# Kernel tuning notes

Hardware: AMD Instinct MI355X
Metric: run time of the kernel (lower is better)

## Reference

```python
import jax, jax.numpy as jnp
import numpy as np

N_NODES = 100000
N_EDGES = 1600000
NFEAT = 128
NHID = 128


def setup_inputs() -> dict:
    key = jax.random.key(0)
    k1, k2, k3, k4 = jax.random.split(key, 4)
    x = jax.random.normal(k1, (N_NODES, NFEAT), dtype=jnp.float32)
    edge_index = jax.random.randint(k2, (2, N_EDGES), 0, N_NODES, dtype=jnp.int64)
    # GCNConv params (glorot-style scale)
    W1 = jax.random.normal(k3, (NFEAT, NHID), dtype=jnp.float32) * (1.0 / np.sqrt(NFEAT))
    b1 = jnp.zeros((NHID,), dtype=jnp.float32)
    return {"x": x, "edge_index": edge_index, "W1": W1, "b1": b1}


def gcn_conv(x, edge_index, W, b):
    # PyG GCNConv: out = D^{-1/2} (A + I) D^{-1/2} (x W) + b
    n = x.shape[0]
    loop = jnp.arange(n, dtype=edge_index.dtype)
    src = jnp.concatenate([edge_index[0], loop])  # message sources
    dst = jnp.concatenate([edge_index[1], loop])  # aggregation targets
    deg = jax.ops.segment_sum(jnp.ones_like(dst, dtype=x.dtype), dst, num_segments=n)
    dinv = jnp.where(deg > 0, jax.lax.rsqrt(deg), 0.0)
    norm = dinv[src] * dinv[dst]  # [E+N]
    h = x @ W  # [N, nhid]
    msg = h[src] * norm[:, None]  # gather + scale, [E+N, nhid]
    out = jax.ops.segment_sum(msg, dst, num_segments=n) + b
    return out


def reference(x, edge_index, W1, b1):
    # forward = gc1(x, edge_index) followed by dropout (identity in eval mode)
    return gcn_conv(x, edge_index, W1, b1)
```

## Files before the change

kernel.cpp:

```cpp
#include <hip/hip_runtime.h>
#include <math.h>


#define N_NODES 100000
#define N_EDGES 1600000
#define NF 128
#define LDW 136

#define BSHIFT 7
#define BNODES 128
#define NBUCK 782
#define ECAP 2432
#define CHUNK 4096
#define NCHUNK 391
#define GEMM_BLOCKS 1563

typedef short bf16x8 __attribute__((ext_vector_type(8)));
typedef float f32x4  __attribute__((ext_vector_type(4)));
typedef unsigned short u16;

__device__ inline u16 f2bf(float f) {
    unsigned int u = __float_as_uint(f);
    return (u16)((u + 0x7fffu + ((u >> 16) & 1u)) >> 16);
}

__device__ inline f32x4 unpk4u(unsigned int u) {
    f32x4 r;
    r[0] = (float)(u & 0xffu);
    r[1] = (float)((u >> 8) & 0xffu);
    r[2] = (float)((u >> 16) & 0xffu);
    r[3] = (float)(u >> 24);
    return r;
}

__global__ __launch_bounds__(256) void prep_kernel(const float* __restrict__ W,
                                                   u16* __restrict__ Wimg,
                                                   int* __restrict__ bcur) {
    const int t = threadIdx.x;
    if (blockIdx.x == 0)
        for (int b = t; b < NBUCK; b += 256) bcur[b] = 0;
    for (int idx = blockIdx.x * 256 + t; idx < NF * NF; idx += 16 * 256) {
        int n = idx >> 7, k = idx & 127;
        Wimg[n * LDW + k] = f2bf(W[k * NF + n]);
    }
}

__global__ __launch_bounds__(256, 4) void fused1_kernel(const float* __restrict__ x,
                                                        const u16* __restrict__ Wimg,
                                                        signed char* __restrict__ h8,
                                                        float* __restrict__ rscale,
                                                        const int* __restrict__ ei,
                                                        int* __restrict__ bcur,
                                                        unsigned int* __restrict__ ebuf) {
    __shared__ __align__(16) char smem[39040];
    const int t = threadIdx.x;

    if (blockIdx.x < NCHUNK) {
        unsigned int* ed = (unsigned int*)smem;
        unsigned int* es = (unsigned int*)(smem + 16384);
        int* cnt = (int*)(smem + 32768);
        int* cur = (int*)(smem + 32768 + 3136);
        const int c = blockIdx.x;
        for (int b = t; b < NBUCK; b += 256) cnt[b] = 0;
        const int e0 = c * CHUNK;
        #pragma unroll 4
        for (int it = 0; it < CHUNK / 256; ++it) {
            int k = it * 256 + t, e = e0 + k;
            if (e < N_EDGES) {
                ed[k] = (unsigned int)ei[N_EDGES + e];
                es[k] = (unsigned int)ei[e];
            } else ed[k] = 0xFFFFFFFFu;
        }
        __syncthreads();
        #pragma unroll 4
        for (int it = 0; it < CHUNK / 256; ++it) {
            unsigned int d = ed[it * 256 + t];
            if (d != 0xFFFFFFFFu) atomicAdd(&cnt[d >> BSHIFT], 1);
        }
        __syncthreads();
        for (int b = t; b < NBUCK; b += 256) {
            int v = cnt[b];
            cur[b] = b * ECAP + (v ? atomicAdd(&bcur[b], v) : 0);
        }
        __syncthreads();
        #pragma unroll 4
        for (int it = 0; it < CHUNK / 256; ++it) {
            int k = it * 256 + t;
            unsigned int d = ed[k];
            if (d != 0xFFFFFFFFu) {
                int pos = atomicAdd(&cur[d >> BSHIFT], 1);
                ebuf[pos] = ((d & (BNODES - 1u)) << 17) | es[k];
            }
        }
        return;
    }

    const int gb = blockIdx.x - NCHUNK;
    const int lane = t & 63;
    const int w = t >> 6;
    const int quad = lane >> 4;
    const int m = lane & 15;
    const int rowbase = gb * 64;
    const int r0 = w * 16;
    const int arow = rowbase + r0 + m;
    const bool rv = arow < N_NODES;
    const float4* x4 = (const float4*)x;

    u16* Wt = (u16*)smem;
    for (int idx = t; idx < (NF * LDW * 2) / 16; idx += 256)
        ((uint4*)Wt)[idx] = ((const uint4*)Wimg)[idx];

    float4 xr[8];
    #pragma unroll
    for (int kt = 0; kt < 4; ++kt) {
        if (rv) {
            xr[2 * kt]     = x4[arow * 32 + kt * 8 + quad * 2];
            xr[2 * kt + 1] = x4[arow * 32 + kt * 8 + quad * 2 + 1];
        } else {
            xr[2 * kt] = make_float4(0.f, 0.f, 0.f, 0.f);
            xr[2 * kt + 1] = make_float4(0.f, 0.f, 0.f, 0.f);
        }
    }
    __syncthreads();

    f32x4 acc[8];
    #pragma unroll
    for (int nt = 0; nt < 8; ++nt) acc[nt] = (f32x4){0.f, 0.f, 0.f, 0.f};

    #pragma unroll
    for (int kt = 0; kt < 4; ++kt) {
        bf16x8 a;
        a[0] = (short)f2bf(xr[2 * kt].x);     a[1] = (short)f2bf(xr[2 * kt].y);
        a[2] = (short)f2bf(xr[2 * kt].z);     a[3] = (short)f2bf(xr[2 * kt].w);
        a[4] = (short)f2bf(xr[2 * kt + 1].x); a[5] = (short)f2bf(xr[2 * kt + 1].y);
        a[6] = (short)f2bf(xr[2 * kt + 1].z); a[7] = (short)f2bf(xr[2 * kt + 1].w);
        #pragma unroll
        for (int nt = 0; nt < 8; ++nt) {
            bf16x8 bb = *(const bf16x8*)&Wt[(nt * 16 + m) * LDW + kt * 32 + quad * 8];
            acc[nt] = __builtin_amdgcn_mfma_f32_16x16x32_bf16(a, bb, acc[nt], 0, 0, 0);
        }
    }

    float rmax[4];
    #pragma unroll
    for (int r = 0; r < 4; ++r) {
        float mx = 0.f;
        #pragma unroll
        for (int nt = 0; nt < 8; ++nt) mx = fmaxf(mx, fabsf(acc[nt][r]));
        #pragma unroll
        for (int off = 1; off < 16; off <<= 1) mx = fmaxf(mx, __shfl_xor(mx, off));
        rmax[r] = fmaxf(mx, 1e-20f);
    }

    __syncthreads();
    char* xs8 = smem;
    #pragma unroll
    for (int r = 0; r < 4; ++r) {
        const float inv = 127.f / rmax[r];
        const int row = r0 + quad * 4 + r;
        #pragma unroll
        for (int nt = 0; nt < 8; ++nt) {
            int q = __float2int_rn(acc[nt][r] * inv) + 128;
            xs8[row * 144 + nt * 16 + m] = (char)q;
        }
        if (m == 0) {
            int grow = rowbase + row;
            if (grow < N_NODES) rscale[grow] = rmax[r] * (1.f / 127.f);
        }
    }
    __syncthreads();

    for (int it = 0; it < 2; ++it) {
        int linear = it * 256 + t;
        int row = linear >> 3, seg = linear & 7;
        int grow = rowbase + row;
        if (grow < N_NODES) {
            uint4 v = *(const uint4*)&xs8[row * 144 + seg * 16];
            ((uint4*)h8)[grow * 8 + seg] = v;
        }
    }
}

__global__ __launch_bounds__(256) void fill3_kernel(unsigned int* __restrict__ ebuf,
                                                    const int* __restrict__ bcur,
                                                    const float* __restrict__ rscale,
                                                    float* __restrict__ combo,
                                                    int4* __restrict__ nodetab) {
    __shared__ unsigned int lde[ECAP];
    __shared__ int lcnt[BNODES];
    __shared__ int lsc[BNODES];
    __shared__ int lcur[BNODES];
    const int t = threadIdx.x, bkt = blockIdx.x;
    const int cnt = min(bcur[bkt], ECAP);
    const int gbase = bkt * ECAP;
    if (t < BNODES) lcnt[t] = 0;
    __syncthreads();
    for (int e = t; e < cnt; e += 256) {
        unsigned int p = ebuf[gbase + e];
        lde[e] = p;
        atomicAdd(&lcnt[p >> 17], 1);
    }
    __syncthreads();
    if (t < BNODES) lsc[t] = lcnt[t];
    __syncthreads();
    #pragma unroll
    for (int off = 1; off < BNODES; off <<= 1) {
        int v = (t < BNODES) ? lsc[t] : 0;
        int add = (t >= off && t < BNODES) ? lsc[t - off] : 0;
        __syncthreads();
        if (t < BNODES) lsc[t] = v + add;
        __syncthreads();
    }
    if (t < BNODES) {
        int c = lcnt[t];
        int startp = gbase + lsc[t] - c;
        lcur[t] = startp;
        int n = (bkt << BSHIFT) + t;
        if (n < N_NODES) {
            float dv = rsqrtf((float)c + 1.0f);
            float cb = dv * rscale[n];
            combo[n] = cb;
            nodetab[n] = make_int4(startp, c, __float_as_int(dv), __float_as_int(cb));
        }
    }
    __syncthreads();
    for (int e = t; e < cnt; e += 256) {
        unsigned int p = lde[e];
        int pos = atomicAdd(&lcur[p >> 17], 1);
        ebuf[pos] = p & 0x1ffffu;
    }
}

__global__ __launch_bounds__(256) void agg_kernel(const signed char* __restrict__ h8,
                                                  const float* __restrict__ combo,
                                                  const int4* __restrict__ nodetab,
                                                  const unsigned int* __restrict__ slot,
                                                  const float* __restrict__ b,
                                                  float* __restrict__ out) {
    const int wave = threadIdx.x >> 6;
    const int lane = threadIdx.x & 63;
    const int i = blockIdx.x * 4 + wave;
    if (i >= N_NODES) return;

    const int4 ni = nodetab[i];
    const int start = ni.x;
    const int m = ni.y;
    const float di = __int_as_float(ni.z);
    const float ci = __int_as_float(ni.w);
    const int half = lane >> 5;
    const int col = lane & 31;

    const unsigned int* h4 = (const unsigned int*)h8;
    f32x4 acc0 = {0.f, 0.f, 0.f, 0.f};
    f32x4 acc1 = {0.f, 0.f, 0.f, 0.f};
    float ws = 0.f;

    for (int base = 0; base < m; base += 64) {
        const int mm = min(m - base, 64);
        int   s_l  = (lane < mm) ? (int)slot[start + base + lane] : 0;
        float cw_l = (lane < mm) ? combo[s_l] : 0.0f;
        const int mu = (mm + 7) & ~7;
        for (int j = 0; j < mu; j += 8) {
            int sj0 = __shfl(s_l, j + 0 + half);
            int sj1 = __shfl(s_l, j + 2 + half);
            int sj2 = __shfl(s_l, j + 4 + half);
            int sj3 = __shfl(s_l, j + 6 + half);
            float wj0 = __shfl(cw_l, j + 0 + half);
            float wj1 = __shfl(cw_l, j + 2 + half);
            float wj2 = __shfl(cw_l, j + 4 + half);
            float wj3 = __shfl(cw_l, j + 6 + half);
            unsigned int u0 = h4[sj0 * 32 + col];
            unsigned int u1 = h4[sj1 * 32 + col];
            unsigned int u2 = h4[sj2 * 32 + col];
            unsigned int u3 = h4[sj3 * 32 + col];
            ws += wj0 + wj1 + wj2 + wj3;
            acc0 += unpk4u(u0) * wj0;
            acc1 += unpk4u(u1) * wj1;
            acc0 += unpk4u(u2) * wj2;
            acc1 += unpk4u(u3) * wj3;
        }
    }

    f32x4 acc = acc0 + acc1;
    #pragma unroll
    for (int c = 0; c < 4; ++c) acc[c] += __shfl_xor(acc[c], 32);
    ws += __shfl_xor(ws, 32);

    if (lane < 32) {
        unsigned int uv = h4[i * 32 + col];
        f32x4 hv = unpk4u(uv);
        float4 bb = ((const float4*)b)[col];
        const float corr = 128.f * (ws + ci);
        float4 o;
        o.x = bb.x + di * (acc[0] + ci * hv[0] - corr);
        o.y = bb.y + di * (acc[1] + ci * hv[1] - corr);
        o.z = bb.z + di * (acc[2] + ci * hv[2] - corr);
        o.w = bb.w + di * (acc[3] + ci * hv[3] - corr);
        ((float4*)out)[i * 32 + col] = o;
    }
}

extern "C" void kernel_launch(void* const* d_in, const int* in_sizes, int n_in,
                              void* d_out, int out_size, void* d_ws, size_t ws_size,
                              hipStream_t stream) {
    const float* x  = (const float*)d_in[0];
    const int*   ei = (const int*)d_in[1];
    const float* W  = (const float*)d_in[2];
    const float* b  = (const float*)d_in[3];
    float* out = (float*)d_out;

    signed char* h8 = (signed char*)d_ws;
    float* rscale = (float*)d_ws + 3300000;
    float* combo  = (float*)d_ws + 3500000;
    int4*  nodetab = (int4*)((int*)d_ws + 3700000);
    int*   bcur   = (int*)d_ws + 4150000;
    u16*   Wimg   = (u16*)((int*)d_ws + 4200000);
    unsigned int* ebuf = (unsigned int*)d_ws + 4300000;

    prep_kernel<<<16, 256, 0, stream>>>(W, Wimg, bcur);
    fused1_kernel<<<NCHUNK + GEMM_BLOCKS, 256, 0, stream>>>(x, Wimg, h8, rscale,
                                                            ei, bcur, ebuf);
    fill3_kernel<<<NBUCK, 256, 0, stream>>>(ebuf, bcur, rscale, combo, nodetab);
    agg_kernel<<<(N_NODES + 3) / 4, 256, 0, stream>>>(h8, combo, nodetab, ebuf, b, out);
}
```

Before: 191.9 us.

## Precompute per-edge source weights into interleaved slot buffer, split fill kernel

Node degrees are now counted with global atomics during edge bucketing. The fill stage is split into two kernels: one prefix-scans degrees to build the node table, the other sorts the edges in place and writes (source, combo weight) pairs. The aggregation kernel then reads the weight next to each source index, which removes its dependent random gather of combo per edge. In exchange there are 1.6M extra global atomics, a memset, one more kernel launch, a doubled slot stride and a smaller bucket capacity (ECAP), which raises the overflow risk for crowded buckets.

```diff
diff --git a/kernel.cpp b/kernel.cpp
--- a/kernel.cpp
+++ b/kernel.cpp
@@ -10,7 +10,7 @@
 #define BSHIFT 7
 #define BNODES 128
 #define NBUCK 782
-#define ECAP 2432
+#define ECAP 2304
 #define CHUNK 4096
 #define NCHUNK 391
 #define GEMM_BLOCKS 1563
@@ -51,7 +51,8 @@
                                                         float* __restrict__ rscale,
                                                         const int* __restrict__ ei,
                                                         int* __restrict__ bcur,
-                                                        unsigned int* __restrict__ ebuf) {
+                                                        int* __restrict__ deg,
+                                                        unsigned int* __restrict__ buf) {
     __shared__ __align__(16) char smem[39040];
     const int t = threadIdx.x;
 
@@ -75,12 +76,15 @@
         #pragma unroll 4
         for (int it = 0; it < CHUNK / 256; ++it) {
             unsigned int d = ed[it * 256 + t];
-            if (d != 0xFFFFFFFFu) atomicAdd(&cnt[d >> BSHIFT], 1);
+            if (d != 0xFFFFFFFFu) {
+                atomicAdd(&cnt[d >> BSHIFT], 1);
+                atomicAdd(&deg[d], 1);
+            }
         }
         __syncthreads();
         for (int b = t; b < NBUCK; b += 256) {
             int v = cnt[b];
-            cur[b] = b * ECAP + (v ? atomicAdd(&bcur[b], v) : 0);
+            cur[b] = b * 2 * ECAP + (v ? atomicAdd(&bcur[b], v) : 0);
         }
         __syncthreads();
         #pragma unroll 4
@@ -89,7 +93,7 @@
             unsigned int d = ed[k];
             if (d != 0xFFFFFFFFu) {
                 int pos = atomicAdd(&cur[d >> BSHIFT], 1);
-                ebuf[pos] = ((d & (BNODES - 1u)) << 17) | es[k];
+                buf[pos] = ((d & (BNODES - 1u)) << 17) | es[k];
             }
         }
         return;
@@ -181,60 +185,61 @@
     }
 }
 
-__global__ __launch_bounds__(256) void fill3_kernel(unsigned int* __restrict__ ebuf,
-                                                    const int* __restrict__ bcur,
-                                                    const float* __restrict__ rscale,
-                                                    float* __restrict__ combo,
-                                                    int4* __restrict__ nodetab) {
+__global__ __launch_bounds__(128) void fill3a_kernel(const int* __restrict__ deg,
+                                                     const float* __restrict__ rscale,
+                                                     float* __restrict__ combo,
+                                                     int4* __restrict__ nodetab) {
+    __shared__ int lsc[BNODES];
+    const int t = threadIdx.x, bkt = blockIdx.x;
+    const int n = (bkt << BSHIFT) + t;
+    const int c = (n < N_NODES) ? deg[n] : 0;
+    lsc[t] = c;
+    __syncthreads();
+    #pragma unroll
+    for (int off = 1; off < BNODES; off <<= 1) {
+        int v = lsc[t];
+        int add = (t >= off) ? lsc[t - off] : 0;
+        __syncthreads();
+        lsc[t] = v + add;
+        __syncthreads();
+    }
+    if (n < N_NODES) {
+        const int startp = bkt * ECAP + lsc[t] - c;
+        float dv = rsqrtf((float)c + 1.0f);
+        float cb = dv * rscale[n];
+        combo[n] = cb;
+        nodetab[n] = make_int4(startp, c, __float_as_int(dv), __float_as_int(cb));
+    }
+}
+
+__global__ __launch_bounds__(256) void fill3b_kernel(unsigned int* __restrict__ buf,
+                                                     const int* __restrict__ bcur,
+                                                     const float* __restrict__ combo,
+                                                     const int4* __restrict__ nodetab) {
     __shared__ unsigned int lde[ECAP];
-    __shared__ int lcnt[BNODES];
-    __shared__ int lsc[BNODES];
     __shared__ int lcur[BNODES];
     const int t = threadIdx.x, bkt = blockIdx.x;
+    if (t < BNODES) {
+        int n = (bkt << BSHIFT) + t;
+        lcur[t] = (n < N_NODES) ? nodetab[n].x : 0;
+    }
     const int cnt = min(bcur[bkt], ECAP);
-    const int gbase = bkt * ECAP;
-    if (t < BNODES) lcnt[t] = 0;
-    __syncthreads();
-    for (int e = t; e < cnt; e += 256) {
-        unsigned int p = ebuf[gbase + e];
-        lde[e] = p;
-        atomicAdd(&lcnt[p >> 17], 1);
-    }
-    __syncthreads();
-    if (t < BNODES) lsc[t] = lcnt[t];
-    __syncthreads();
-    #pragma unroll
-    for (int off = 1; off < BNODES; off <<= 1) {
-        int v = (t < BNODES) ? lsc[t] : 0;
-        int add = (t >= off && t < BNODES) ? lsc[t - off] : 0;
-        __syncthreads();
-        if (t < BNODES) lsc[t] = v + add;
-        __syncthreads();
-    }
-    if (t < BNODES) {
-        int c = lcnt[t];
-        int startp = gbase + lsc[t] - c;
-        lcur[t] = startp;
-        int n = (bkt << BSHIFT) + t;
-        if (n < N_NODES) {
-            float dv = rsqrtf((float)c + 1.0f);
-            float cb = dv * rscale[n];
-            combo[n] = cb;
-            nodetab[n] = make_int4(startp, c, __float_as_int(dv), __float_as_int(cb));
-        }
-    }
-    __syncthreads();
+    const int rbase = bkt * 2 * ECAP;
+    for (int e = t; e < cnt; e += 256) lde[e] = buf[rbase + e];
+    __syncthreads();
+    uint2* sw = (uint2*)buf;
     for (int e = t; e < cnt; e += 256) {
         unsigned int p = lde[e];
+        unsigned int src = p & 0x1ffffu;
+        float w = combo[src];
         int pos = atomicAdd(&lcur[p >> 17], 1);
-        ebuf[pos] = p & 0x1ffffu;
+        sw[pos] = make_uint2(src, __float_as_uint(w));
     }
 }
 
 __global__ __launch_bounds__(256) void agg_kernel(const signed char* __restrict__ h8,
-                                                  const float* __restrict__ combo,
                                                   const int4* __restrict__ nodetab,
-                                                  const unsigned int* __restrict__ slot,
+                                                  const uint2* __restrict__ slotw,
                                                   const float* __restrict__ b,
                                                   float* __restrict__ out) {
     const int wave = threadIdx.x >> 6;
@@ -257,8 +262,9 @@
 
     for (int base = 0; base < m; base += 64) {
         const int mm = min(m - base, 64);
-        int   s_l  = (lane < mm) ? (int)slot[start + base + lane] : 0;
-        float cw_l = (lane < mm) ? combo[s_l] : 0.0f;
+        uint2 swv = (lane < mm) ? slotw[start + base + lane] : make_uint2(0u, 0u);
+        int   s_l  = (int)swv.x;
+        float cw_l = __uint_as_float(swv.y);
         const int mu = (mm + 7) & ~7;
         for (int j = 0; j < mu; j += 8) {
             int sj0 = __shfl(s_l, j + 0 + half);
@@ -311,15 +317,19 @@
 
     signed char* h8 = (signed char*)d_ws;
     float* rscale = (float*)d_ws + 3300000;
-    float* combo  = (float*)d_ws + 3500000;
-    int4*  nodetab = (int4*)((int*)d_ws + 3700000);
-    int*   bcur   = (int*)d_ws + 4150000;
-    u16*   Wimg   = (u16*)((int*)d_ws + 4200000);
-    unsigned int* ebuf = (unsigned int*)d_ws + 4300000;
-
+    float* combo  = (float*)d_ws + 3450000;
+    int4*  nodetab = (int4*)((int*)d_ws + 3600000);
+    int*   deg    = (int*)d_ws + 4020000;
+    int*   bcur   = (int*)d_ws + 4130000;
+    u16*   Wimg   = (u16*)((int*)d_ws + 4140000);
+    unsigned int* buf = (unsigned int*)d_ws + 4150000;
+
+    hipMemsetAsync(deg, 0, N_NODES * sizeof(int), stream);
     prep_kernel<<<16, 256, 0, stream>>>(W, Wimg, bcur);
     fused1_kernel<<<NCHUNK + GEMM_BLOCKS, 256, 0, stream>>>(x, Wimg, h8, rscale,
-                                                            ei, bcur, ebuf);
-    fill3_kernel<<<NBUCK, 256, 0, stream>>>(ebuf, bcur, rscale, combo, nodetab);
-    agg_kernel<<<(N_NODES + 3) / 4, 256, 0, stream>>>(h8, combo, nodetab, ebuf, b, out);
-}
+                                                            ei, bcur, deg, buf);
+    fill3a_kernel<<<NBUCK, 128, 0, stream>>>(deg, rscale, combo, nodetab);
+    fill3b_kernel<<<NBUCK, 256, 0, stream>>>(buf, bcur, combo, nodetab);
+    agg_kernel<<<(N_NODES + 3) / 4, 256, 0, stream>>>(h8, nodetab,
+                                                      (const uint2*)buf, b, out);
+}
```

After: 257.7 us. 1.34x slower.

## Fuse per-bucket edge sort into aggregation kernel using shared-memory slot lists

Applied to the files above, without the earlier changes.

Replaces the fill3 kernel, which sorted edges into global memory and wrote a node table, with a light kernel that only counts degrees and computes combo weights. The aggregation kernel now handles one half-bucket of 64 nodes per block. It re-reads the bucket's edges, counting-sorts them into shared memory, then each wave aggregates 16 nodes from the local slot list. This removes the global scatter write and the nodetab round trip. In exchange, ebuf is read several times, each block gets far fewer independent waves (1564 blocks instead of 25000), and any half-bucket with more than HCAP edges is silently truncated.

```diff
diff --git a/kernel.cpp b/kernel.cpp
--- a/kernel.cpp
+++ b/kernel.cpp
@@ -11,6 +11,7 @@
 #define BNODES 128
 #define NBUCK 782
 #define ECAP 2432
+#define HCAP 1536
 #define CHUNK 4096
 #define NCHUNK 391
 #define GEMM_BLOCKS 1563
@@ -181,122 +182,137 @@
     }
 }
 
-__global__ __launch_bounds__(256) void fill3_kernel(unsigned int* __restrict__ ebuf,
-                                                    const int* __restrict__ bcur,
-                                                    const float* __restrict__ rscale,
-                                                    float* __restrict__ combo,
-                                                    int4* __restrict__ nodetab) {
-    __shared__ unsigned int lde[ECAP];
+__global__ __launch_bounds__(256) void comboK_kernel(const unsigned int* __restrict__ ebuf,
+                                                     const int* __restrict__ bcur,
+                                                     const float* __restrict__ rscale,
+                                                     float* __restrict__ combo) {
     __shared__ int lcnt[BNODES];
-    __shared__ int lsc[BNODES];
-    __shared__ int lcur[BNODES];
     const int t = threadIdx.x, bkt = blockIdx.x;
+    if (t < BNODES) lcnt[t] = 0;
+    __syncthreads();
     const int cnt = min(bcur[bkt], ECAP);
-    const int gbase = bkt * ECAP;
-    if (t < BNODES) lcnt[t] = 0;
+    for (int e = t; e < cnt; e += 256)
+        atomicAdd(&lcnt[ebuf[bkt * ECAP + e] >> 17], 1);
+    __syncthreads();
+    if (t < BNODES) {
+        int n = (bkt << BSHIFT) + t;
+        if (n < N_NODES)
+            combo[n] = rsqrtf((float)lcnt[t] + 1.0f) * rscale[n];
+    }
+}
+
+__global__ __launch_bounds__(256) void aggB_kernel(const unsigned int* __restrict__ ebuf,
+                                                   const int* __restrict__ bcur,
+                                                   const float* __restrict__ rscale,
+                                                   const float* __restrict__ combo,
+                                                   const signed char* __restrict__ h8,
+                                                   const float* __restrict__ b,
+                                                   float* __restrict__ out) {
+    __shared__ unsigned int lslot[HCAP];
+    __shared__ int lcnt[64];
+    __shared__ int lbase[64];
+    __shared__ int lcur[64];
+    const int t = threadIdx.x;
+    const int bkt = blockIdx.x >> 1;
+    const int hb  = blockIdx.x & 1;
+    const int n0  = (bkt << BSHIFT) + hb * 64;
+    const unsigned lo = (unsigned)(hb * 64), hi = lo + 64u;
+    const int cnt = min(bcur[bkt], ECAP);
+    const int rbase = bkt * ECAP;
+
+    if (t < 64) lcnt[t] = 0;
     __syncthreads();
     for (int e = t; e < cnt; e += 256) {
-        unsigned int p = ebuf[gbase + e];
-        lde[e] = p;
-        atomicAdd(&lcnt[p >> 17], 1);
-    }
-    __syncthreads();
-    if (t < BNODES) lsc[t] = lcnt[t];
-    __syncthreads();
-    #pragma unroll
-    for (int off = 1; off < BNODES; off <<= 1) {
-        int v = (t < BNODES) ? lsc[t] : 0;
-        int add = (t >= off && t < BNODES) ? lsc[t - off] : 0;
-        __syncthreads();
-        if (t < BNODES) lsc[t] = v + add;
-        __syncthreads();
-    }
-    if (t < BNODES) {
-        int c = lcnt[t];
-        int startp = gbase + lsc[t] - c;
-        lcur[t] = startp;
-        int n = (bkt << BSHIFT) + t;
-        if (n < N_NODES) {
-            float dv = rsqrtf((float)c + 1.0f);
-            float cb = dv * rscale[n];
-            combo[n] = cb;
-            nodetab[n] = make_int4(startp, c, __float_as_int(dv), __float_as_int(cb));
-        }
+        unsigned p = ebuf[rbase + e];
+        unsigned ld = p >> 17;
+        if (ld >= lo && ld < hi) atomicAdd(&lcnt[ld - lo], 1);
+    }
+    __syncthreads();
+    if (t < 64) {
+        int v = lcnt[t];
+        int s = v;
+        #pragma unroll
+        for (int off = 1; off < 64; off <<= 1) {
+            int u = __shfl_up(s, off);
+            if (t >= off) s += u;
+        }
+        lbase[t] = s - v;
+        lcur[t]  = s - v;
     }
     __syncthreads();
     for (int e = t; e < cnt; e += 256) {
-        unsigned int p = lde[e];
-        int pos = atomicAdd(&lcur[p >> 17], 1);
-        ebuf[pos] = p & 0x1ffffu;
-    }
-}
-
-__global__ __launch_bounds__(256) void agg_kernel(const signed char* __restrict__ h8,
-                                                  const float* __restrict__ combo,
-                                                  const int4* __restrict__ nodetab,
-                                                  const unsigned int* __restrict__ slot,
-                                                  const float* __restrict__ b,
-                                                  float* __restrict__ out) {
-    const int wave = threadIdx.x >> 6;
-    const int lane = threadIdx.x & 63;
-    const int i = blockIdx.x * 4 + wave;
-    if (i >= N_NODES) return;
-
-    const int4 ni = nodetab[i];
-    const int start = ni.x;
-    const int m = ni.y;
-    const float di = __int_as_float(ni.z);
-    const float ci = __int_as_float(ni.w);
+        unsigned p = ebuf[rbase + e];
+        unsigned ld = p >> 17;
+        if (ld >= lo && ld < hi) {
+            int pos = atomicAdd(&lcur[ld - lo], 1);
+            if (pos < HCAP) lslot[pos] = p & 0x1ffffu;
+        }
+    }
+    __syncthreads();
+
+    const int wave = t >> 6;
+    const int lane = t & 63;
     const int half = lane >> 5;
-    const int col = lane & 31;
-
+    const int col  = lane & 31;
     const unsigned int* h4 = (const unsigned int*)h8;
-    f32x4 acc0 = {0.f, 0.f, 0.f, 0.f};
-    f32x4 acc1 = {0.f, 0.f, 0.f, 0.f};
-    float ws = 0.f;
-
-    for (int base = 0; base < m; base += 64) {
-        const int mm = min(m - base, 64);
-        int   s_l  = (lane < mm) ? (int)slot[start + base + lane] : 0;
-        float cw_l = (lane < mm) ? combo[s_l] : 0.0f;
-        const int mu = (mm + 7) & ~7;
-        for (int j = 0; j < mu; j += 8) {
-            int sj0 = __shfl(s_l, j + 0 + half);
-            int sj1 = __shfl(s_l, j + 2 + half);
-            int sj2 = __shfl(s_l, j + 4 + half);
-            int sj3 = __shfl(s_l, j + 6 + half);
-            float wj0 = __shfl(cw_l, j + 0 + half);
-            float wj1 = __shfl(cw_l, j + 2 + half);
-            float wj2 = __shfl(cw_l, j + 4 + half);
-            float wj3 = __shfl(cw_l, j + 6 + half);
-            unsigned int u0 = h4[sj0 * 32 + col];
-            unsigned int u1 = h4[sj1 * 32 + col];
-            unsigned int u2 = h4[sj2 * 32 + col];
-            unsigned int u3 = h4[sj3 * 32 + col];
-            ws += wj0 + wj1 + wj2 + wj3;
-            acc0 += unpk4u(u0) * wj0;
-            acc1 += unpk4u(u1) * wj1;
-            acc0 += unpk4u(u2) * wj2;
-            acc1 += unpk4u(u3) * wj3;
-        }
-    }
-
-    f32x4 acc = acc0 + acc1;
-    #pragma unroll
-    for (int c = 0; c < 4; ++c) acc[c] += __shfl_xor(acc[c], 32);
-    ws += __shfl_xor(ws, 32);
-
-    if (lane < 32) {
-        unsigned int uv = h4[i * 32 + col];
-        f32x4 hv = unpk4u(uv);
-        float4 bb = ((const float4*)b)[col];
-        const float corr = 128.f * (ws + ci);
-        float4 o;
-        o.x = bb.x + di * (acc[0] + ci * hv[0] - corr);
-        o.y = bb.y + di * (acc[1] + ci * hv[1] - corr);
-        o.z = bb.z + di * (acc[2] + ci * hv[2] - corr);
-        o.w = bb.w + di * (acc[3] + ci * hv[3] - corr);
-        ((float4*)out)[i * 32 + col] = o;
+    float4 bb = make_float4(0.f, 0.f, 0.f, 0.f);
+    if (lane < 32) bb = ((const float4*)b)[col];
+
+    for (int nn = 0; nn < 16; ++nn) {
+        const int li = wave * 16 + nn;
+        const int i  = n0 + li;
+        if (i >= N_NODES) continue;
+        const int start = lbase[li];
+        const int m     = lcnt[li];
+        const float di  = rsqrtf((float)m + 1.0f);
+        const float ci  = di * rscale[i];
+
+        f32x4 acc0 = {0.f, 0.f, 0.f, 0.f};
+        f32x4 acc1 = {0.f, 0.f, 0.f, 0.f};
+        float ws = 0.f;
+
+        for (int base = 0; base < m; base += 64) {
+            const int mm = min(m - base, 64);
+            int   s_l  = (lane < mm) ? (int)lslot[start + base + lane] : 0;
+            float cw_l = (lane < mm) ? combo[s_l] : 0.0f;
+            const int mu = (mm + 7) & ~7;
+            for (int j = 0; j < mu; j += 8) {
+                int sj0 = __shfl(s_l, j + 0 + half);
+                int sj1 = __shfl(s_l, j + 2 + half);
+                int sj2 = __shfl(s_l, j + 4 + half);
+                int sj3 = __shfl(s_l, j + 6 + half);
+                float wj0 = __shfl(cw_l, j + 0 + half);
+                float wj1 = __shfl(cw_l, j + 2 + half);
+                float wj2 = __shfl(cw_l, j + 4 + half);
+                float wj3 = __shfl(cw_l, j + 6 + half);
+                unsigned int u0 = h4[sj0 * 32 + col];
+                unsigned int u1 = h4[sj1 * 32 + col];
+                unsigned int u2 = h4[sj2 * 32 + col];
+                unsigned int u3 = h4[sj3 * 32 + col];
+                ws += wj0 + wj1 + wj2 + wj3;
+                acc0 += unpk4u(u0) * wj0;
+                acc1 += unpk4u(u1) * wj1;
+                acc0 += unpk4u(u2) * wj2;
+                acc1 += unpk4u(u3) * wj3;
+            }
+        }
+
+        f32x4 acc = acc0 + acc1;
+        #pragma unroll
+        for (int c = 0; c < 4; ++c) acc[c] += __shfl_xor(acc[c], 32);
+        ws += __shfl_xor(ws, 32);
+
+        if (lane < 32) {
+            unsigned int uv = h4[i * 32 + col];
+            f32x4 hv = unpk4u(uv);
+            const float corr = 128.f * (ws + ci);
+            float4 o;
+            o.x = bb.x + di * (acc[0] + ci * hv[0] - corr);
+            o.y = bb.y + di * (acc[1] + ci * hv[1] - corr);
+            o.z = bb.z + di * (acc[2] + ci * hv[2] - corr);
+            o.w = bb.w + di * (acc[3] + ci * hv[3] - corr);
+            ((float4*)out)[i * 32 + col] = o;
+        }
     }
 }
 
@@ -311,15 +327,14 @@
 
     signed char* h8 = (signed char*)d_ws;
     float* rscale = (float*)d_ws + 3300000;
-    float* combo  = (float*)d_ws + 3500000;
-    int4*  nodetab = (int4*)((int*)d_ws + 3700000);
-    int*   bcur   = (int*)d_ws + 4150000;
-    u16*   Wimg   = (u16*)((int*)d_ws + 4200000);
+    float* combo  = (float*)d_ws + 3450000;
+    int*   bcur   = (int*)d_ws + 4130000;
+    u16*   Wimg   = (u16*)((int*)d_ws + 4140000);
     unsigned int* ebuf = (unsigned int*)d_ws + 4300000;
 
     prep_kernel<<<16, 256, 0, stream>>>(W, Wimg, bcur);
     fused1_kernel<<<NCHUNK + GEMM_BLOCKS, 256, 0, stream>>>(x, Wimg, h8, rscale,
                                                             ei, bcur, ebuf);
-    fill3_kernel<<<NBUCK, 256, 0, stream>>>(ebuf, bcur, rscale, combo, nodetab);
-    agg_kernel<<<(N_NODES + 3) / 4, 256, 0, stream>>>(h8, combo, nodetab, ebuf, b, out);
-}
+    comboK_kernel<<<NBUCK, 256, 0, stream>>>(ebuf, bcur, rscale, combo);
+    aggB_kernel<<<NBUCK * 2, 256, 0, stream>>>(ebuf, bcur, rscale, combo, h8, b, out);
+}
```

Result: no change. 191.1 us (-0.5%).
